# Kernel tuning notes

Measured on AMD Instinct MI355X. Metric: run time of the kernel, lower is better.

## Reference

```python
import jax, jax.numpy as jnp
import numpy as np

B, S, D = 32, 512, 512      # batch, seq_len, d_model
H, K = 16, 32               # head_num, head_dim
A = 256                     # attention_hidden_dim


def setup_inputs() -> dict:
    key = jax.random.key(0)
    ks = jax.random.split(key, 10)
    s = lambda fan_in: 1.0 / np.sqrt(fan_in)
    return {
        "x":   jax.random.normal(ks[0], (B, S, D), dtype=jnp.float32),
        # per-head Q projections: Linear(D, D), stored [H, in, out]
        "Qw":  jax.random.normal(ks[1], (H, D, D), dtype=jnp.float32) * s(D),
        "Qb":  jax.random.normal(ks[2], (H, D), dtype=jnp.float32) * s(D),
        # per-head V projections: Linear(D, K)
        "Vw":  jax.random.normal(ks[3], (H, D, K), dtype=jnp.float32) * s(D),
        "Vb":  jax.random.normal(ks[4], (H, K), dtype=jnp.float32) * s(D),
        # additive attention pooling: Linear(H*K, A) then Linear(A, 1)
        "Wv":  jax.random.normal(ks[5], (H * K, A), dtype=jnp.float32) * s(H * K),
        "bv":  jax.random.normal(ks[6], (A,), dtype=jnp.float32) * s(H * K),
        "wq":  jax.random.normal(ks[7], (A, 1), dtype=jnp.float32) * s(A),
        "bq":  jax.random.normal(ks[8], (1,), dtype=jnp.float32) * s(A),
    }


def reference(x, Qw, Qb, Vw, Vb, Wv, bv, wq, bq):
    # per-head query projection: [B, H, S, D]
    q = jnp.einsum("bsd,hde->bhse", x, Qw) + Qb[None, :, None, :]
    # raw scores: [B, H, S, S] (s = query pos, t = key pos)
    scores = jnp.einsum("bhse,bte->bhst", q, x)
    # NOTE: softmax over dim=-2 (the QUERY axis), not the usual key axis
    attn = jax.nn.softmax(scores, axis=-2)
    # context: [B, H, S, D]
    ctx = jnp.einsum("bhst,btd->bhsd", attn, x)
    # per-head value projection then concat heads -> [B, S, H*K]
    head_out = jnp.einsum("bhsd,hdk->bshk", ctx, Vw) + Vb[None, None, :, :]
    h = head_out.reshape(B, S, H * K)
    # dropout is identity at inference
    # additive attention pooling
    a = jnp.tanh(h @ Wv + bv) @ wq + bq          # [B, S, 1]
    z = jnp.einsum("bs,bsk->bk", a[..., 0], h)   # [B, H*K]
    return z
```

## Files before the change

### kernel.cpp

```cpp
#include <hip/hip_runtime.h>

#define DEVFN __device__ __forceinline__

typedef _Float16 f16;
typedef _Float16 f16x8 __attribute__((ext_vector_type(8)));
typedef _Float16 f16x4 __attribute__((ext_vector_type(4)));
typedef _Float16 f16x2 __attribute__((ext_vector_type(2)));
typedef float    f32x4 __attribute__((ext_vector_type(4)));

enum { NB = 32, NS = 512, ND = 512, NH = 16, NK = 32, NA = 256 };

#define SZ(x) ((size_t)(x))

typedef __attribute__((address_space(3))) void       as3_void;
typedef const __attribute__((address_space(1))) void as1_cvoid;
DEVFN void ldsdma16(const void* g, void* l) {
  __builtin_amdgcn_global_load_lds((as1_cvoid*)g, (as3_void*)l, 16, 0, 0);
}

DEVFN int xcd_swz(int flat, int n) {
  return (flat & 7) * (n >> 3) + (flat >> 3);
}

DEVFN void gemm_core_128(const f16* __restrict__ Ag, const f16* __restrict__ Bg,
                         int lda, int ldb, int nk, f16* lds, f32x4 acc[4][4]) {
  f16* As = lds;
  f16* Bs = lds + 128 * 64;
  const int tid  = threadIdx.x;
  const int lane = tid & 63;
  const int wvid = tid >> 6, wr = wvid >> 1, wc = wvid & 1;
  const int srow = tid >> 3, scol = (tid & 7) * 8;
  const int frow = lane & 15, fk = (lane >> 4) * 8;
  for (int ks = 0; ks < nk; ++ks) {
    const f16* ga = Ag + ks * 64 + scol;
    const f16* gb = Bg + ks * 64 + scol;
#pragma unroll
    for (int r = 0; r < 4; ++r) {
      ldsdma16(ga + SZ(r * 32 + srow) * lda, As + SZ(r * 32 + srow) * 64 + scol);
      ldsdma16(gb + SZ(r * 32 + srow) * ldb, Bs + SZ(r * 32 + srow) * 64 + scol);
    }
    __syncthreads();
#pragma unroll
    for (int kk = 0; kk < 64; kk += 32) {
      f16x8 a[4], b[4];
#pragma unroll
      for (int i = 0; i < 4; ++i)
        a[i] = *(const f16x8*)(As + SZ(wr * 64 + i * 16 + frow) * 64 + kk + fk);
#pragma unroll
      for (int j = 0; j < 4; ++j)
        b[j] = *(const f16x8*)(Bs + SZ(wc * 64 + j * 16 + frow) * 64 + kk + fk);
#pragma unroll
      for (int i = 0; i < 4; ++i)
#pragma unroll
        for (int j = 0; j < 4; ++j)
          acc[i][j] = __builtin_amdgcn_mfma_f32_16x16x32_f16(a[i], b[j], acc[i][j], 0, 0, 0);
    }
    __syncthreads();
  }
}

DEVFN void wlds_write(f16* wlds, int row, int col, f16 v) {
  int byte = (row * 256 + col * 2) ^ ((row & 7) << 4);
  *(f16*)((char*)wlds + byte) = v;
}
DEVFN f16x8 wlds_read8(const f16* wlds, int row, int col ) {
  int byte = (row * 256 + col * 2) ^ ((row & 7) << 4);
  return *(const f16x8*)((const char*)wlds + byte);
}

__global__ __launch_bounds__(256) void k_cast4(const float* __restrict__ s,
                                               f16* __restrict__ d, int n4) {
  int i = blockIdx.x * 256 + threadIdx.x;
  if (i >= n4) return;
  float4 v = ((const float4*)s)[i];
  f16x4 o; o[0] = (f16)v.x; o[1] = (f16)v.y; o[2] = (f16)v.z; o[3] = (f16)v.w;
  ((f16x4*)d)[i] = o;
}

__global__ void k_tcast(const float* __restrict__ src, f16* __restrict__ dst,
                        int R, int C, long sStride, long dStride) {
  __shared__ float tile[32][33];
  src += (long)blockIdx.z * sStride;
  dst += (long)blockIdx.z * dStride;
  int c0 = blockIdx.x * 32, r0 = blockIdx.y * 32;
  int tx = threadIdx.x, ty = threadIdx.y;
#pragma unroll
  for (int i = 0; i < 4; ++i)
    tile[ty + 8 * i][tx] = src[(long)(r0 + ty + 8 * i) * C + c0 + tx];
  __syncthreads();
#pragma unroll
  for (int i = 0; i < 4; ++i)
    dst[(long)(c0 + ty + 8 * i) * R + r0 + tx] = (f16)tile[tx][ty + 8 * i];
}

__global__ __launch_bounds__(256) void k_gemm_xv(const f16* __restrict__ xh,
                                                 const f16* __restrict__ vwt,
                                                 f16* __restrict__ xvt) {
  __shared__ f16 smem[128 * 64 * 2];
  int z = blockIdx.z, b = z >> 2, hg = z & 3, tm = blockIdx.x;
  f32x4 acc[4][4] = {};
  gemm_core_128(xh + SZ(b) * NS * ND + SZ(tm) * 128 * ND,
                vwt + SZ(hg) * 4 * NK * ND, ND, ND, ND / 64, smem, acc);
  int tid = threadIdx.x, lane = tid & 63, wvid = tid >> 6, wr = wvid >> 1, wc = wvid & 1;
  int rbase = (lane >> 4) * 4, cbase = lane & 15;
#pragma unroll
  for (int mi = 0; mi < 4; ++mi)
#pragma unroll
    for (int ni = 0; ni < 4; ++ni) {
      int n = wc * 64 + ni * 16 + cbase;
      int hh = hg * 4 + (n >> 5), kk = n & 31;
#pragma unroll
      for (int r = 0; r < 4; ++r) {
        int t = tm * 128 + wr * 64 + mi * 16 + rbase + r;
        xvt[(SZ(b * NH + hh) * NK + kk) * NS + t] = (f16)acc[mi][ni][r];
      }
    }
}

__global__ __launch_bounds__(256) void k_gemm_q(const f16* __restrict__ xh,
                                                const f16* __restrict__ qwt,
                                                const float* __restrict__ Qb,
                                                f16* __restrict__ qc, int b0) {
  __shared__ f16 smem[128 * 64 * 2];
  int n = gridDim.x * gridDim.y * gridDim.z;
  int flat = blockIdx.x + gridDim.x * (blockIdx.y + gridDim.y * blockIdx.z);
  int lg = xcd_swz(flat, n);
  int tm = lg & 3, tn = (lg >> 2) & 3, bhl = lg >> 4;
  int b = b0 + (bhl >> 4), h = bhl & 15;
  f32x4 acc[4][4] = {};
  gemm_core_128(xh + SZ(b) * NS * ND + SZ(tm) * 128 * ND,
                qwt + SZ(h) * ND * ND + SZ(tn) * 128 * ND, ND, ND, ND / 64, smem, acc);
  int tid = threadIdx.x, lane = tid & 63, wvid = tid >> 6, wr = wvid >> 1, wc = wvid & 1;
  int rbase = (lane >> 4) * 4, cbase = lane & 15;
  f16* qb = qc + SZ(bhl) * NS * ND;
#pragma unroll
  for (int mi = 0; mi < 4; ++mi)
#pragma unroll
    for (int ni = 0; ni < 4; ++ni) {
      int colg = tn * 128 + wc * 64 + ni * 16 + cbase;
      float bias = Qb[h * ND + colg];
#pragma unroll
      for (int r = 0; r < 4; ++r) {
        int rowg = tm * 128 + wr * 64 + mi * 16 + rbase + r;
        qb[SZ(rowg) * ND + colg] = (f16)(acc[mi][ni][r] + bias);
      }
    }
}

__global__ __launch_bounds__(256) void k_scores_stats(const f16* __restrict__ qc,
                                                      const f16* __restrict__ xh,
                                                      f16* __restrict__ sc,
                                                      float* __restrict__ mp,
                                                      float* __restrict__ zp, int b0) {
  __shared__ f16 smem[128 * 64 * 2];
  int n = gridDim.x * gridDim.y * gridDim.z;
  int flat = blockIdx.x + gridDim.x * (blockIdx.y + gridDim.y * blockIdx.z);
  int lg = xcd_swz(flat, n);
  int st = lg & 3, tt = (lg >> 2) & 3, bhl = lg >> 4;
  int b = b0 + (bhl >> 4);
  f32x4 acc[4][4] = {};
  gemm_core_128(qc + SZ(bhl) * NS * ND + SZ(st) * 128 * ND,
                xh + SZ(b) * NS * ND + SZ(tt) * 128 * ND, ND, ND, ND / 64, smem, acc);
  int tid = threadIdx.x, lane = tid & 63, wvid = tid >> 6, wr = wvid >> 1, wc = wvid & 1;
  float* sbuf = (float*)smem;

  float mh[4];
#pragma unroll
  for (int ni = 0; ni < 4; ++ni) {
    float m = -1e30f;
#pragma unroll
    for (int mi = 0; mi < 4; ++mi)
#pragma unroll
      for (int r = 0; r < 4; ++r) m = fmaxf(m, acc[mi][ni][r]);
    m = fmaxf(m, __shfl_xor(m, 16));
    m = fmaxf(m, __shfl_xor(m, 32));
    mh[ni] = m;
  }
  if (lane < 16) {
#pragma unroll
    for (int ni = 0; ni < 4; ++ni)
      sbuf[wr * 128 + wc * 64 + ni * 16 + lane] = mh[ni];
  }
  __syncthreads();
  int cbase = lane & 15;
  float tmc[4];
#pragma unroll
  for (int ni = 0; ni < 4; ++ni) {
    int col = wc * 64 + ni * 16 + cbase;
    tmc[ni] = fmaxf(sbuf[col], sbuf[128 + col]);
  }
  f16* scb = sc + (SZ(bhl * 4 + st) * 4 + tt) * (128 * 128);
  float sm[4];
#pragma unroll
  for (int ni = 0; ni < 4; ++ni) sm[ni] = 0.f;
#pragma unroll
  for (int mi = 0; mi < 4; ++mi) {
#pragma unroll
    for (int ni = 0; ni < 4; ++ni) {
      f16x4 o;
#pragma unroll
      for (int r = 0; r < 4; ++r) {
        float ev = __expf(acc[mi][ni][r] - tmc[ni]);
        o[r] = (f16)ev;
        sm[ni] += ev;
      }
      ((f16x4*)(scb + (mi * 4 + ni) * 1024))[tid] = o;
    }
  }
#pragma unroll
  for (int ni = 0; ni < 4; ++ni) {
    sm[ni] += __shfl_xor(sm[ni], 16);
    sm[ni] += __shfl_xor(sm[ni], 32);
  }
  if (lane < 16) {
#pragma unroll
    for (int ni = 0; ni < 4; ++ni)
      sbuf[256 + wr * 128 + wc * 64 + ni * 16 + lane] = sm[ni];
  }
  __syncthreads();
  if (tid < 128) {
    float m  = fmaxf(sbuf[tid], sbuf[128 + tid]);
    float zz = sbuf[256 + tid] + sbuf[384 + tid];
    size_t idx = (SZ(bhl) * 4 + st) * NS + tt * 128 + tid;
    mp[idx] = m; zp[idx] = zz;
  }
}

__global__ __launch_bounds__(256) void k_stats_combine(const float* __restrict__ mp,
                                                       const float* __restrict__ zp,
                                                       float* __restrict__ cs) {
  int i = blockIdx.x * 256 + threadIdx.x;
  int bhl = i >> 9, t = i & (NS - 1);
  float mv[4], m = -1e30f;
#pragma unroll
  for (int st = 0; st < 4; ++st) {
    mv[st] = mp[(SZ(bhl) * 4 + st) * NS + t];
    m = fmaxf(m, mv[st]);
  }
  float es[4], Z = 0.f;
#pragma unroll
  for (int st = 0; st < 4; ++st) {
    es[st] = __expf(mv[st] - m);
    Z += zp[(SZ(bhl) * 4 + st) * NS + t] * es[st];
  }
  float rZ = 1.0f / Z;
#pragma unroll
  for (int st = 0; st < 4; ++st)
    cs[(SZ(bhl) * 4 + st) * NS + t] = es[st] * rZ;
}

__global__ __launch_bounds__(256) void k_norm_pv(const f16* __restrict__ sc,
                                                 const f16* __restrict__ xvt,
                                                 const float* __restrict__ cs,
                                                 const float* __restrict__ Vb,
                                                 f16* __restrict__ h16, int b0) {
  __shared__ f16 wlds[128 * 128];
  int bhl = blockIdx.y, b = b0 + (bhl >> 4), h = bhl & 15;
  int st = blockIdx.x;
  int tid = threadIdx.x, lane = tid & 63, wvid = tid >> 6, wr = wvid >> 1, wc = wvid & 1;
  int rbase = (lane >> 4) * 4, cbase = lane & 15, fk = (lane >> 4) * 8;
  f32x4 acc2[2][2] = {};
  const f16* xvh = xvt + SZ(b * NH + h) * NK * NS;
  for (int tt = 0; tt < 4; ++tt) {
    const f16* scb = sc + (SZ(bhl * 4 + st) * 4 + tt) * (128 * 128);
#pragma unroll
    for (int ni = 0; ni < 4; ++ni) {
      int tl = wc * 64 + ni * 16 + cbase;
      float csv = cs[(SZ(bhl) * 4 + st) * NS + tt * 128 + tl];
#pragma unroll
      for (int mi = 0; mi < 4; ++mi) {
        f16x4 v = ((const f16x4*)(scb + (mi * 4 + ni) * 1024))[tid];
#pragma unroll
        for (int r = 0; r < 4; ++r) {
          int sl = wr * 64 + mi * 16 + rbase + r;
          wlds_write(wlds, sl, tl, (f16)((float)v[r] * csv));
        }
      }
    }
    __syncthreads();
    const f16* xvb = xvh + tt * 128;
#pragma unroll
    for (int tc = 0; tc < 4; ++tc) {
      f16x8 aw[2], bx[2];
#pragma unroll
      for (int m2 = 0; m2 < 2; ++m2)
        aw[m2] = wlds_read8(wlds, wvid * 32 + m2 * 16 + cbase, tc * 32 + fk);
#pragma unroll
      for (int n2 = 0; n2 < 2; ++n2)
        bx[n2] = *(const f16x8*)(xvb + SZ(n2 * 16 + cbase) * NS + tc * 32 + fk);
#pragma unroll
      for (int m2 = 0; m2 < 2; ++m2)
#pragma unroll
        for (int n2 = 0; n2 < 2; ++n2)
          acc2[m2][n2] = __builtin_amdgcn_mfma_f32_16x16x32_f16(aw[m2], bx[n2], acc2[m2][n2], 0, 0, 0);
    }
    __syncthreads();
  }
  const float* vb = Vb + h * NK;
#pragma unroll
  for (int m2 = 0; m2 < 2; ++m2)
#pragma unroll
    for (int n2 = 0; n2 < 2; ++n2)
#pragma unroll
      for (int r = 0; r < 4; ++r) {
        int sg = st * 128 + wvid * 32 + m2 * 16 + rbase + r;
        int kk = n2 * 16 + cbase;
        float val = acc2[m2][n2][r] + vb[kk];
        h16[SZ(b * NS + sg) * (NH * NK) + h * NK + kk] = (f16)val;
      }
}

__global__ __launch_bounds__(256) void k_gemm_u(const f16* __restrict__ h16,
                                                const f16* __restrict__ wvt,
                                                const float* __restrict__ bv,
                                                f16* __restrict__ U) {
  __shared__ f16 smem[128 * 64 * 2];
  int tm = blockIdx.x, tn = blockIdx.y;
  f32x4 acc[4][4] = {};
  gemm_core_128(h16 + SZ(tm) * 128 * ND, wvt + SZ(tn) * 128 * ND, ND, ND, ND / 64, smem, acc);
  int tid = threadIdx.x, lane = tid & 63, wvid = tid >> 6, wr = wvid >> 1, wc = wvid & 1;
  int rbase = (lane >> 4) * 4, cbase = lane & 15;
#pragma unroll
  for (int mi = 0; mi < 4; ++mi)
#pragma unroll
    for (int ni = 0; ni < 4; ++ni) {
      int colg = tn * 128 + wc * 64 + ni * 16 + cbase;
      float bias = bv[colg];
#pragma unroll
      for (int r = 0; r < 4; ++r) {
        int rowg = tm * 128 + wr * 64 + mi * 16 + rbase + r;
        U[SZ(rowg) * NA + colg] = (f16)tanhf(acc[mi][ni][r] + bias);
      }
    }
}

__global__ __launch_bounds__(256) void k_a(const f16* __restrict__ U,
                                           const float* __restrict__ wq,
                                           const float* __restrict__ bq,
                                           float* __restrict__ a) {
  int wid = (blockIdx.x * 256 + threadIdx.x) >> 6;
  int lane = threadIdx.x & 63;
  const f16* u = U + SZ(wid) * NA;
  float p = 0.f;
#pragma unroll
  for (int j = 0; j < NA / 64; ++j) p += (float)u[lane + 64 * j] * wq[lane + 64 * j];
#pragma unroll
  for (int o = 32; o; o >>= 1) p += __shfl_xor(p, o);
  if (lane == 0) a[wid] = p + bq[0];
}

__global__ __launch_bounds__(256) void k_zpart(const f16* __restrict__ h16,
                                               const float* __restrict__ a,
                                               float* __restrict__ zpt) {
  int b = blockIdx.y, c = blockIdx.x, tid = threadIdx.x;
  float z0 = 0.f, z1 = 0.f;
  for (int s = 0; s < 64; ++s) {
    int sg = c * 64 + s;
    float av = a[b * NS + sg];
    const f16* hr = h16 + SZ(b * NS + sg) * (NH * NK);
    f16x2 v = ((const f16x2*)hr)[tid];
    z0 += av * (float)v[0];
    z1 += av * (float)v[1];
  }
  zpt[SZ(b * 8 + c) * 512 + 2 * tid]     = z0;
  zpt[SZ(b * 8 + c) * 512 + 2 * tid + 1] = z1;
}

__global__ __launch_bounds__(256) void k_zred(const float* __restrict__ zpt,
                                              float* __restrict__ out) {
  int i = blockIdx.x * 256 + threadIdx.x;
  int b = i >> 9, k = i & 511;
  float z = 0.f;
#pragma unroll
  for (int c = 0; c < 8; ++c) z += zpt[SZ(b * 8 + c) * 512 + k];
  out[i] = z;
}

static size_t ws_plan(int cb, size_t off[14]) {
  size_t o = 0;
  auto put = [&](size_t bytes) { size_t r = o; o += (bytes + 255) & ~SZ(255); return r; };
  off[0]  = put(SZ(NB) * NS * ND * 2);
  off[1]  = put(SZ(NH) * ND * ND * 2);
  off[2]  = put(SZ(NA) * ND * 2);
  off[3]  = put(SZ(NH) * NK * ND * 2);
  off[4]  = put(SZ(NB) * NH * NK * NS * 2);
  off[5]  = put(SZ(cb) * NH * NS * ND * 2);
  off[6]  = put(SZ(cb) * NH * NS * NS * 2);
  off[7]  = put(SZ(cb) * NH * 4 * NS * 4);
  off[8]  = put(SZ(cb) * NH * 4 * NS * 4);
  off[9]  = put(SZ(cb) * NH * 4 * NS * 4);
  off[10] = put(SZ(NB) * NS * NH * NK * 2);
  off[11] = put(SZ(NB) * NS * NA * 2);
  off[12] = put(SZ(NB) * NS * 4);
  off[13] = put(SZ(NB) * 8 * NH * NK * 4);
  return o;
}

extern "C" void kernel_launch(void* const* d_in, const int* in_sizes, int n_in,
                              void* d_out, int out_size, void* d_ws, size_t ws_size,
                              hipStream_t stream) {
  const float* x  = (const float*)d_in[0];
  const float* Qw = (const float*)d_in[1];
  const float* Qb = (const float*)d_in[2];
  const float* Vw = (const float*)d_in[3];
  const float* Vb = (const float*)d_in[4];
  const float* Wv = (const float*)d_in[5];
  const float* bv = (const float*)d_in[6];
  const float* wq = (const float*)d_in[7];
  const float* bq = (const float*)d_in[8];

  int cbv = 0;
  size_t off[14];
  const int cand[5] = {32, 16, 8, 4, 2};
  for (int ci = 0; ci < 5; ++ci) {
    if (ws_plan(cand[ci], off) <= ws_size) { cbv = cand[ci]; break; }
  }
  if (cbv == 0) return;

  char* ws = (char*)d_ws;
  f16*   xh   = (f16*)(ws + off[0]);
  f16*   qwt  = (f16*)(ws + off[1]);
  f16*   wvt  = (f16*)(ws + off[2]);
  f16*   vwt  = (f16*)(ws + off[3]);
  f16*   xvt  = (f16*)(ws + off[4]);
  f16*   qc   = (f16*)(ws + off[5]);
  f16*   sc   = (f16*)(ws + off[6]);
  float* mp   = (float*)(ws + off[7]);
  float* zps  = (float*)(ws + off[8]);
  float* cs   = (float*)(ws + off[9]);
  f16*   h16  = (f16*)(ws + off[10]);
  f16*   U    = (f16*)(ws + off[11]);
  float* a    = (float*)(ws + off[12]);
  float* zpt  = (float*)(ws + off[13]);
  float* zout = (float*)d_out;

  k_cast4<<<SZ(NB) * NS * ND / 4 / 256, 256, 0, stream>>>(x, xh, NB * NS * ND / 4);
  k_tcast<<<dim3(16, 16, 16), dim3(32, 8), 0, stream>>>(Qw, qwt, ND, ND, (long)ND * ND, (long)ND * ND);
  k_tcast<<<dim3(8, 16, 1), dim3(32, 8), 0, stream>>>(Wv, wvt, ND, NA, 0, 0);
  k_tcast<<<dim3(1, 16, 16), dim3(32, 8), 0, stream>>>(Vw, vwt, ND, NK, (long)ND * NK, (long)NK * ND);
  k_gemm_xv<<<dim3(4, 1, NB * 4), 256, 0, stream>>>(xh, vwt, xvt);

  for (int b0 = 0; b0 < NB; b0 += cbv) {
    k_gemm_q<<<dim3(4, 4, cbv * NH), 256, 0, stream>>>(xh, qwt, Qb, qc, b0);
    k_scores_stats<<<dim3(4, 4, cbv * NH), 256, 0, stream>>>(qc, xh, sc, mp, zps, b0);
    k_stats_combine<<<cbv * NH * NS / 256, 256, 0, stream>>>(mp, zps, cs);
    k_norm_pv<<<dim3(4, cbv * NH), 256, 0, stream>>>(sc, xvt, cs, Vb, h16, b0);
  }

  k_gemm_u<<<dim3(NB * NS / 128, 2, 1), 256, 0, stream>>>(h16, wvt, bv, U);
  k_a<<<NB * NS / 4, 256, 0, stream>>>(U, wq, bq, a);
  k_zpart<<<dim3(8, NB), 256, 0, stream>>>(h16, a, zpt);
  k_zred<<<NB * 512 / 256, 256, 0, stream>>>(zpt, zout);
}
```

Measured before the change: 573.5 us.

## Use 256x256 tiles with a 4-stage LDS-DMA pipeline for Q and score GEMMs

Replaces the 128x128 single-buffered GEMM core in the Q-projection and score kernels with a 256x256 tile, 512-thread core. It keeps four LDS stages of K=32 slices in flight, using explicit vmcnt waits, swizzled LDS reads and raised wave priority around the MFMA block. The larger tile roughly halves global operand traffic per FLOP and hides load latency behind compute. The score layout and softmax statistics change from 4 to 2 partial row blocks, so stats_combine and norm_pv are rewritten to index the new layout. In exchange it uses 128 KB of LDS per block and many more accumulator registers, which limits occupancy.

```diff
diff --git a/kernel.cpp b/kernel.cpp
--- a/kernel.cpp
+++ b/kernel.cpp
@@ -20,6 +20,62 @@
 
 DEVFN int xcd_swz(int flat, int n) {
   return (flat & 7) * (n >> 3) + (flat >> 3);
+}
+
+DEVFN void gemm256_pipe(const f16* __restrict__ Ag, const f16* __restrict__ Bg,
+                        int lda, int ldb, f16* smem, f32x4 acc[8][4]) {
+  const int tid  = threadIdx.x;
+  const int lane = tid & 63;
+  const int wid  = tid >> 6;
+  const int wr   = wid >> 2;
+  const int wcn  = wid & 3;
+  const int s_r    = tid >> 2;
+  const int s_gsrc = (tid & 3) ^ (s_r & 3);
+  const int frow = lane & 15;
+  const int fg   = lane >> 4;
+
+  auto stage = [&](int t) {
+    f16* buf = smem + (t & 3) * 16384;
+    const f16* As = Ag + t * 32;
+    const f16* Bs = Bg + t * 32;
+#pragma unroll
+    for (int j = 0; j < 2; ++j)
+      ldsdma16(As + SZ(j * 128 + s_r) * lda + s_gsrc * 8, buf + j * 4096 + tid * 8);
+#pragma unroll
+    for (int j = 0; j < 2; ++j)
+      ldsdma16(Bs + SZ(j * 128 + s_r) * ldb + s_gsrc * 8, buf + 8192 + j * 4096 + tid * 8);
+  };
+
+  stage(0); stage(1); stage(2);
+
+  for (int t = 0; t < 16; ++t) {
+    if (t <= 13)      asm volatile("s_waitcnt vmcnt(8)" ::: "memory");
+    else if (t == 14) asm volatile("s_waitcnt vmcnt(4)" ::: "memory");
+    else              asm volatile("s_waitcnt vmcnt(0)" ::: "memory");
+    __builtin_amdgcn_s_barrier();
+    if (t < 13) stage(t + 3);
+
+    const f16* bufA = smem + (t & 3) * 16384;
+    const f16* bufB = bufA + 8192;
+    f16x8 af[8], bf[4];
+#pragma unroll
+    for (int mi = 0; mi < 8; ++mi) {
+      int r_ = wr * 128 + mi * 16 + frow;
+      af[mi] = *(const f16x8*)(bufA + r_ * 32 + ((fg ^ (r_ & 3)) * 8));
+    }
+#pragma unroll
+    for (int ni = 0; ni < 4; ++ni) {
+      int r_ = wcn * 64 + ni * 16 + frow;
+      bf[ni] = *(const f16x8*)(bufB + r_ * 32 + ((fg ^ (r_ & 3)) * 8));
+    }
+    __builtin_amdgcn_s_setprio(1);
+#pragma unroll
+    for (int mi = 0; mi < 8; ++mi)
+#pragma unroll
+      for (int ni = 0; ni < 4; ++ni)
+        acc[mi][ni] = __builtin_amdgcn_mfma_f32_16x16x32_f16(af[mi], bf[ni], acc[mi][ni], 0, 0, 0);
+    __builtin_amdgcn_s_setprio(0);
+  }
 }
 
 DEVFN void gemm_core_128(const f16* __restrict__ Ag, const f16* __restrict__ Bg,
@@ -63,7 +119,7 @@
   int byte = (row * 256 + col * 2) ^ ((row & 7) << 4);
   *(f16*)((char*)wlds + byte) = v;
 }
-DEVFN f16x8 wlds_read8(const f16* wlds, int row, int col ) {
+DEVFN f16x8 wlds_read8(const f16* wlds, int row, int col) {
   int byte = (row * 256 + col * 2) ^ ((row & 7) << 4);
   return *(const f16x8*)((const char*)wlds + byte);
 }
@@ -117,51 +173,52 @@
     }
 }
 
-__global__ __launch_bounds__(256) void k_gemm_q(const f16* __restrict__ xh,
-                                                const f16* __restrict__ qwt,
-                                                const float* __restrict__ Qb,
-                                                f16* __restrict__ qc, int b0) {
-  __shared__ f16 smem[128 * 64 * 2];
-  int n = gridDim.x * gridDim.y * gridDim.z;
-  int flat = blockIdx.x + gridDim.x * (blockIdx.y + gridDim.y * blockIdx.z);
-  int lg = xcd_swz(flat, n);
-  int tm = lg & 3, tn = (lg >> 2) & 3, bhl = lg >> 4;
+__global__ __launch_bounds__(512, 2) void k_gemm_q256(const f16* __restrict__ xh,
+                                                      const f16* __restrict__ qwt,
+                                                      const float* __restrict__ Qb,
+                                                      f16* __restrict__ qc, int b0) {
+  __shared__ f16 smem[65536];
+  int n = gridDim.x;
+  int lg = xcd_swz(blockIdx.x, n);
+  int tm2 = lg & 1, tn2 = (lg >> 1) & 1, bhl = lg >> 2;
   int b = b0 + (bhl >> 4), h = bhl & 15;
-  f32x4 acc[4][4] = {};
-  gemm_core_128(xh + SZ(b) * NS * ND + SZ(tm) * 128 * ND,
-                qwt + SZ(h) * ND * ND + SZ(tn) * 128 * ND, ND, ND, ND / 64, smem, acc);
-  int tid = threadIdx.x, lane = tid & 63, wvid = tid >> 6, wr = wvid >> 1, wc = wvid & 1;
+  f32x4 acc[8][4] = {};
+  gemm256_pipe(xh + SZ(b) * NS * ND + SZ(tm2) * 256 * ND,
+               qwt + SZ(h) * ND * ND + SZ(tn2) * 256 * ND, ND, ND, smem, acc);
+  int lane = threadIdx.x & 63, wid = threadIdx.x >> 6;
+  int wr = wid >> 2, wcn = wid & 3;
   int rbase = (lane >> 4) * 4, cbase = lane & 15;
   f16* qb = qc + SZ(bhl) * NS * ND;
 #pragma unroll
-  for (int mi = 0; mi < 4; ++mi)
+  for (int mi = 0; mi < 8; ++mi)
 #pragma unroll
     for (int ni = 0; ni < 4; ++ni) {
-      int colg = tn * 128 + wc * 64 + ni * 16 + cbase;
+      int colg = tn2 * 256 + wcn * 64 + ni * 16 + cbase;
       float bias = Qb[h * ND + colg];
 #pragma unroll
       for (int r = 0; r < 4; ++r) {
-        int rowg = tm * 128 + wr * 64 + mi * 16 + rbase + r;
+        int rowg = tm2 * 256 + wr * 128 + mi * 16 + rbase + r;
         qb[SZ(rowg) * ND + colg] = (f16)(acc[mi][ni][r] + bias);
       }
     }
 }
 
-__global__ __launch_bounds__(256) void k_scores_stats(const f16* __restrict__ qc,
+__global__ __launch_bounds__(512, 2) void k_scores256(const f16* __restrict__ qc,
                                                       const f16* __restrict__ xh,
                                                       f16* __restrict__ sc,
                                                       float* __restrict__ mp,
                                                       float* __restrict__ zp, int b0) {
-  __shared__ f16 smem[128 * 64 * 2];
-  int n = gridDim.x * gridDim.y * gridDim.z;
-  int flat = blockIdx.x + gridDim.x * (blockIdx.y + gridDim.y * blockIdx.z);
-  int lg = xcd_swz(flat, n);
-  int st = lg & 3, tt = (lg >> 2) & 3, bhl = lg >> 4;
+  __shared__ f16 smem[65536];
+  int n = gridDim.x;
+  int lg = xcd_swz(blockIdx.x, n);
+  int st2 = lg & 1, tt2 = (lg >> 1) & 1, bhl = lg >> 2;
   int b = b0 + (bhl >> 4);
-  f32x4 acc[4][4] = {};
-  gemm_core_128(qc + SZ(bhl) * NS * ND + SZ(st) * 128 * ND,
-                xh + SZ(b) * NS * ND + SZ(tt) * 128 * ND, ND, ND, ND / 64, smem, acc);
-  int tid = threadIdx.x, lane = tid & 63, wvid = tid >> 6, wr = wvid >> 1, wc = wvid & 1;
+  f32x4 acc[8][4] = {};
+  gemm256_pipe(qc + SZ(bhl) * NS * ND + SZ(st2) * 256 * ND,
+               xh + SZ(b) * NS * ND + SZ(tt2) * 256 * ND, ND, ND, smem, acc);
+  int tid = threadIdx.x, lane = tid & 63, wid = tid >> 6;
+  int wr = wid >> 2, wcn = wid & 3;
+  __syncthreads();
   float* sbuf = (float*)smem;
 
   float mh[4];
@@ -169,7 +226,7 @@
   for (int ni = 0; ni < 4; ++ni) {
     float m = -1e30f;
 #pragma unroll
-    for (int mi = 0; mi < 4; ++mi)
+    for (int mi = 0; mi < 8; ++mi)
 #pragma unroll
       for (int r = 0; r < 4; ++r) m = fmaxf(m, acc[mi][ni][r]);
     m = fmaxf(m, __shfl_xor(m, 16));
@@ -179,22 +236,20 @@
   if (lane < 16) {
 #pragma unroll
     for (int ni = 0; ni < 4; ++ni)
-      sbuf[wr * 128 + wc * 64 + ni * 16 + lane] = mh[ni];
+      sbuf[wr * 256 + wcn * 64 + ni * 16 + lane] = mh[ni];
   }
   __syncthreads();
-  int cbase = lane & 15;
+  int cb_ = lane & 15;
   float tmc[4];
 #pragma unroll
   for (int ni = 0; ni < 4; ++ni) {
-    int col = wc * 64 + ni * 16 + cbase;
-    tmc[ni] = fmaxf(sbuf[col], sbuf[128 + col]);
-  }
-  f16* scb = sc + (SZ(bhl * 4 + st) * 4 + tt) * (128 * 128);
-  float sm[4];
-#pragma unroll
-  for (int ni = 0; ni < 4; ++ni) sm[ni] = 0.f;
-#pragma unroll
-  for (int mi = 0; mi < 4; ++mi) {
+    int col = wcn * 64 + ni * 16 + cb_;
+    tmc[ni] = fmaxf(sbuf[col], sbuf[256 + col]);
+  }
+  f16x4* scb = (f16x4*)(sc + SZ(lg) * 65536);
+  float sm[4] = {0.f, 0.f, 0.f, 0.f};
+#pragma unroll
+  for (int mi = 0; mi < 8; ++mi)
 #pragma unroll
     for (int ni = 0; ni < 4; ++ni) {
       f16x4 o;
@@ -204,9 +259,8 @@
         o[r] = (f16)ev;
         sm[ni] += ev;
       }
-      ((f16x4*)(scb + (mi * 4 + ni) * 1024))[tid] = o;
-    }
-  }
+      scb[((wid * 8 + mi) * 4 + ni) * 64 + lane] = o;
+    }
 #pragma unroll
   for (int ni = 0; ni < 4; ++ni) {
     sm[ni] += __shfl_xor(sm[ni], 16);
@@ -215,13 +269,13 @@
   if (lane < 16) {
 #pragma unroll
     for (int ni = 0; ni < 4; ++ni)
-      sbuf[256 + wr * 128 + wc * 64 + ni * 16 + lane] = sm[ni];
+      sbuf[512 + wr * 256 + wcn * 64 + ni * 16 + lane] = sm[ni];
   }
   __syncthreads();
-  if (tid < 128) {
-    float m  = fmaxf(sbuf[tid], sbuf[128 + tid]);
-    float zz = sbuf[256 + tid] + sbuf[384 + tid];
-    size_t idx = (SZ(bhl) * 4 + st) * NS + tt * 128 + tid;
+  if (tid < 256) {
+    float m  = fmaxf(sbuf[tid], sbuf[256 + tid]);
+    float zz = sbuf[512 + tid] + sbuf[768 + tid];
+    size_t idx = (SZ(bhl) * 2 + st2) * NS + tt2 * 256 + tid;
     mp[idx] = m; zp[idx] = zz;
   }
 }
@@ -231,22 +285,14 @@
                                                        float* __restrict__ cs) {
   int i = blockIdx.x * 256 + threadIdx.x;
   int bhl = i >> 9, t = i & (NS - 1);
-  float mv[4], m = -1e30f;
-#pragma unroll
-  for (int st = 0; st < 4; ++st) {
-    mv[st] = mp[(SZ(bhl) * 4 + st) * NS + t];
-    m = fmaxf(m, mv[st]);
-  }
-  float es[4], Z = 0.f;
-#pragma unroll
-  for (int st = 0; st < 4; ++st) {
-    es[st] = __expf(mv[st] - m);
-    Z += zp[(SZ(bhl) * 4 + st) * NS + t] * es[st];
-  }
+  float m0 = mp[(SZ(bhl) * 2 + 0) * NS + t];
+  float m1 = mp[(SZ(bhl) * 2 + 1) * NS + t];
+  float m = fmaxf(m0, m1);
+  float e0 = __expf(m0 - m), e1 = __expf(m1 - m);
+  float Z = zp[(SZ(bhl) * 2 + 0) * NS + t] * e0 + zp[(SZ(bhl) * 2 + 1) * NS + t] * e1;
   float rZ = 1.0f / Z;
-#pragma unroll
-  for (int st = 0; st < 4; ++st)
-    cs[(SZ(bhl) * 4 + st) * NS + t] = es[st] * rZ;
+  cs[(SZ(bhl) * 2 + 0) * NS + t] = e0 * rZ;
+  cs[(SZ(bhl) * 2 + 1) * NS + t] = e1 * rZ;
 }
 
 __global__ __launch_bounds__(256) void k_norm_pv(const f16* __restrict__ sc,
@@ -262,14 +308,17 @@
   f32x4 acc2[2][2] = {};
   const f16* xvh = xvt + SZ(b * NH + h) * NK * NS;
   for (int tt = 0; tt < 4; ++tt) {
-    const f16* scb = sc + (SZ(bhl * 4 + st) * 4 + tt) * (128 * 128);
+    int blk = (bhl * 2 + (tt >> 1)) * 2 + (st >> 1);
+    const f16x4* scb = (const f16x4*)(sc + SZ(blk) * 65536);
+    int wave_sc = (st & 1) * 4 + ((tt & 1) * 2 + wc);
 #pragma unroll
     for (int ni = 0; ni < 4; ++ni) {
       int tl = wc * 64 + ni * 16 + cbase;
-      float csv = cs[(SZ(bhl) * 4 + st) * NS + tt * 128 + tl];
+      float csv = cs[(SZ(bhl) * 2 + (st >> 1)) * NS + tt * 128 + tl];
 #pragma unroll
       for (int mi = 0; mi < 4; ++mi) {
-        f16x4 v = ((const f16x4*)(scb + (mi * 4 + ni) * 1024))[tid];
+        int mi_sc = wr * 4 + mi;
+        f16x4 v = scb[((wave_sc * 8 + mi_sc) * 4 + ni) * 64 + lane];
 #pragma unroll
         for (int r = 0; r < 4; ++r) {
           int sl = wr * 64 + mi * 16 + rbase + r;
@@ -386,9 +435,9 @@
   off[4]  = put(SZ(NB) * NH * NK * NS * 2);
   off[5]  = put(SZ(cb) * NH * NS * ND * 2);
   off[6]  = put(SZ(cb) * NH * NS * NS * 2);
-  off[7]  = put(SZ(cb) * NH * 4 * NS * 4);
-  off[8]  = put(SZ(cb) * NH * 4 * NS * 4);
-  off[9]  = put(SZ(cb) * NH * 4 * NS * 4);
+  off[7]  = put(SZ(cb) * NH * 2 * NS * 4);
+  off[8]  = put(SZ(cb) * NH * 2 * NS * 4);
+  off[9]  = put(SZ(cb) * NH * 2 * NS * 4);
   off[10] = put(SZ(NB) * NS * NH * NK * 2);
   off[11] = put(SZ(NB) * NS * NA * 2);
   off[12] = put(SZ(NB) * NS * 4);
@@ -441,8 +490,8 @@
   k_gemm_xv<<<dim3(4, 1, NB * 4), 256, 0, stream>>>(xh, vwt, xvt);
 
   for (int b0 = 0; b0 < NB; b0 += cbv) {
-    k_gemm_q<<<dim3(4, 4, cbv * NH), 256, 0, stream>>>(xh, qwt, Qb, qc, b0);
-    k_scores_stats<<<dim3(4, 4, cbv * NH), 256, 0, stream>>>(qc, xh, sc, mp, zps, b0);
+    k_gemm_q256<<<cbv * 64, 512, 0, stream>>>(xh, qwt, Qb, qc, b0);
+    k_scores256<<<cbv * 64, 512, 0, stream>>>(qc, xh, sc, mp, zps, b0);
     k_stats_combine<<<cbv * NH * NS / 256, 256, 0, stream>>>(mp, zps, cs);
     k_norm_pv<<<dim3(4, cbv * NH), 256, 0, stream>>>(sc, xvt, cs, Vb, h16, b0);
   }
```

Measured after the change: 548.2 us. 1.05x faster.
